# Optimization experiments

Hardware: AMD Instinct MI355X
Metric: run time of the kernel (lower is better)

The kernel has to match this reference:

```python
import jax, jax.numpy as jnp
import numpy as np

N = 100000
EPS = 1e-16

def gat_conv(x, edge_index, W, a_src, a_dst, bias, heads, out_c):
    # x: [N, F_in]; W: [F_in, heads*out_c]; a_src/a_dst: [heads, out_c]; bias: [heads*out_c]
    n = x.shape[0]
    loops = jnp.arange(n)
    src = jnp.concatenate([edge_index[0], loops])  # add self loops (PyG default)
    dst = jnp.concatenate([edge_index[1], loops])
    h = (x @ W).reshape(n, heads, out_c)                       # [N,H,C]
    s_src = jnp.sum(h * a_src[None], axis=-1)                  # [N,H]
    s_dst = jnp.sum(h * a_dst[None], axis=-1)                  # [N,H]
    e = jax.nn.leaky_relu(s_src[src] + s_dst[dst], 0.2)        # [E,H]
    m = jax.ops.segment_max(e, dst, num_segments=n)            # [N,H]
    ex = jnp.exp(e - m[dst])
    denom = jax.ops.segment_sum(ex, dst, num_segments=n)       # [N,H]
    alpha = ex / (denom[dst] + EPS)                            # [E,H]
    msg = h[src] * alpha[:, :, None]                           # [E,H,C]
    out = jax.ops.segment_sum(msg, dst, num_segments=n)        # [N,H,C]
    return out.reshape(n, heads * out_c) + bias

def setup_inputs() -> dict:
    key = jax.random.key(0)
    ks = jax.random.split(key, 10)
    num_features, num_classes, H = 512, 10, 8
    E = 3200000
    x = jax.random.normal(ks[0], (N, num_features), dtype=jnp.float32)
    edge_index = jax.random.randint(ks[1], (2, E), 0, N, dtype=jnp.int64)
    g = lambda k, shape, fan: jax.random.normal(k, shape, dtype=jnp.float32) * (1.0 / np.sqrt(fan))
    W1 = g(ks[2], (num_features, H * 8), num_features)
    a_src1 = g(ks[3], (H, 8), 8)
    a_dst1 = g(ks[4], (H, 8), 8)
    b1 = jnp.zeros((H * 8,), dtype=jnp.float32)
    W2 = g(ks[5], (H * 8, H * num_classes), H * 8)
    a_src2 = g(ks[6], (H, num_classes), num_classes)
    a_dst2 = g(ks[7], (H, num_classes), num_classes)
    b2 = jnp.zeros((H * num_classes,), dtype=jnp.float32)
    return {"x": x, "edge_index": edge_index, "W1": W1, "a_src1": a_src1,
            "a_dst1": a_dst1, "b1": b1, "W2": W2, "a_src2": a_src2,
            "a_dst2": a_dst2, "b2": b2}

def reference(x, edge_index, W1, a_src1, a_dst1, b1, W2, a_src2, a_dst2, b2):
    # inference mode: dropout = identity
    h = jax.nn.elu(gat_conv(x, edge_index, W1, a_src1, a_dst1, b1, heads=8, out_c=8))
    out = gat_conv(h, edge_index, W2, a_src2, a_dst2, b2, heads=8, out_c=10)
    return jax.nn.log_softmax(out, axis=1)
```

## Files before the change

### kernel.cpp

```cpp
#include <hip/hip_runtime.h>
#include <math.h>

#define NN 100000
#define NE 3200000
#define FIN 512
#define NH 8
#define C1 8
#define HC1 64
#define C2 10
#define HC2 80

#define EPB 4096
#define NBLK 782
#define NBUK 196
#define SCN (NBUK * NBLK)
#define SCNB 150

typedef unsigned int uint;
using bf16x8 = __attribute__((ext_vector_type(8))) short;
using f32x4  = __attribute__((ext_vector_type(4))) float;

__device__ float g_h1[NN * HC1];
__device__ float g_hact[NN * HC1];
__device__ float g_h2[NN * HC2];
__device__ uint  g_h1b[NN * 32];
__device__ uint  g_h2b[NN * 40];
__device__ uint  g_w1bt[64 * 256];
__device__ float g_ssrc[NN * NH];
__device__ float g_sdst[NN * NH];
__device__ int   g_off[NN + 1];
__device__ uint  g_pscan[SCN];
__device__ uint  g_bsum2[256];
__device__ uint  g_ebuf[NE];
__device__ int   g_csr[NE];

__device__ __forceinline__ float lrelu(float x) { return fmaxf(x, 0.2f * x); }

__device__ __forceinline__ uint bf16_rne(float x) {
  uint u = __float_as_uint(x);
  u += 0x7fffu + ((u >> 16) & 1u);
  return u >> 16;
}
__device__ __forceinline__ uint packbf2(float lo, float hi) {
  return bf16_rne(lo) | (bf16_rne(hi) << 16);
}
__device__ __forceinline__ float blo(uint v) { return __uint_as_float(v << 16); }
__device__ __forceinline__ float bhi(uint v) { return __uint_as_float(v & 0xffff0000u); }

__global__ __launch_bounds__(256) void p1count_kernel(const int* __restrict__ ei) {
  __shared__ uint cnt[NBUK];
  int tid = threadIdx.x;
  for (int i = tid; i < NBUK; i += 256) cnt[i] = 0;
  __syncthreads();
  const int* dstp = ei + NE;
  int base = blockIdx.x * EPB;
#pragma unroll 4
  for (int k = 0; k < 16; k++) {
    int e = base + k * 256 + tid;
    if (e < NE) atomicAdd(&cnt[dstp[e] >> 9], 1u);
  }
  __syncthreads();
  for (int i = tid; i < NBUK; i += 256) g_pscan[i * NBLK + blockIdx.x] = cnt[i];
}

__global__ __launch_bounds__(1024) void scn_block_kernel() {
  __shared__ uint sd[1024];
  int tid = threadIdx.x;
  int i = blockIdx.x * 1024 + tid;
  uint v = (i < SCN) ? g_pscan[i] : 0;
  sd[tid] = v;
  __syncthreads();
  for (int off = 1; off < 1024; off <<= 1) {
    uint x = (tid >= off) ? sd[tid - off] : 0;
    __syncthreads();
    sd[tid] += x;
    __syncthreads();
  }
  if (i < SCN) g_pscan[i] = sd[tid] - v;
  if (tid == 1023) g_bsum2[blockIdx.x] = sd[1023];
}

__global__ void scn_tops_kernel() {
  __shared__ uint sd[256];
  int tid = threadIdx.x;
  uint v = (tid < SCNB) ? g_bsum2[tid] : 0;
  sd[tid] = v;
  __syncthreads();
  for (int off = 1; off < 256; off <<= 1) {
    uint x = (tid >= off) ? sd[tid - off] : 0;
    __syncthreads();
    sd[tid] += x;
    __syncthreads();
  }
  g_bsum2[tid] = sd[tid] - v;
}

__global__ __launch_bounds__(1024) void scn_add_kernel() {
  int i = blockIdx.x * 1024 + threadIdx.x;
  if (i < SCN) g_pscan[i] += g_bsum2[i >> 10];
}

__global__ __launch_bounds__(256) void p1scatter_kernel(const int* __restrict__ ei) {
  __shared__ uint cur[NBUK];
  int tid = threadIdx.x;
  for (int i = tid; i < NBUK; i += 256) cur[i] = g_pscan[i * NBLK + blockIdx.x];
  __syncthreads();
  const int* srcp = ei;
  const int* dstp = ei + NE;
  int base = blockIdx.x * EPB;
#pragma unroll 4
  for (int k = 0; k < 16; k++) {
    int e = base + k * 256 + tid;
    if (e < NE) {
      int d = dstp[e], s = srcp[e];
      uint pos = atomicAdd(&cur[d >> 9], 1u);
      g_ebuf[pos] = ((uint)(d & 511) << 17) | (uint)s;
    }
  }
}

__global__ __launch_bounds__(1024) void p2build_kernel() {
  __shared__ uint hist[512];
  __shared__ uint sc[512];
  __shared__ uint cur[512];
  int tid = threadIdx.x;
  int b = blockIdx.x;
  uint bstart = g_pscan[b * NBLK];
  uint bend = (b < NBUK - 1) ? g_pscan[(b + 1) * NBLK] : NE;
  if (tid < 512) hist[tid] = 0;
  __syncthreads();
  for (uint j = bstart + tid; j < bend; j += 1024)
    atomicAdd(&hist[g_ebuf[j] >> 17], 1u);
  __syncthreads();
  uint v = (tid < 512) ? hist[tid] : 0;
  if (tid < 512) sc[tid] = v;
  __syncthreads();
  for (int off = 1; off < 512; off <<= 1) {
    uint x = (tid < 512 && tid >= off) ? sc[tid - off] : 0;
    __syncthreads();
    if (tid < 512) sc[tid] += x;
    __syncthreads();
  }
  if (tid < 512) {
    uint excl = sc[tid] - v;
    cur[tid] = excl;
    int dst = b * 512 + tid;
    if (dst < NN) g_off[dst] = (int)(bstart + excl);
  }
  if (b == NBUK - 1 && tid == 0) g_off[NN] = NE;
  __syncthreads();
  for (uint j = bstart + tid; j < bend; j += 1024) {
    uint val = g_ebuf[j];
    uint pos = bstart + atomicAdd(&cur[val >> 17], 1u);
    g_csr[pos] = (int)(val & 0x1FFFFu);
  }
}

__global__ __launch_bounds__(256) void w1cast_kernel(const float* __restrict__ W) {
  int idx = blockIdx.x * 256 + threadIdx.x;
  int n = idx & 63, kp = idx >> 6;
  float lo = W[(2 * kp) * HC1 + n];
  float hi = W[(2 * kp + 1) * HC1 + n];
  g_w1bt[n * 256 + kp] = packbf2(lo, hi);
}

__device__ __forceinline__ int sw_idx(int row, int g) {
  return row * 32 + ((g ^ (row & 7)) << 2);
}

__global__ __launch_bounds__(256) void gemm1_kernel(const float* __restrict__ X) {
  __shared__ uint sA[64 * 32];
  __shared__ uint sB[64 * 32];
  int t = threadIdx.x;
  int w = t >> 6, l = t & 63;
  int q = l >> 4, c = l & 15;
  int r0 = blockIdx.x * 64;
  int sr = t >> 2;
  int sc = t & 3;
  int xrow = r0 + sr; if (xrow >= NN) xrow = NN - 1;
  const float* xbase = &X[(long)xrow * FIN + sc * 16];
  const uint* wbase = &g_w1bt[sr * 256 + sc * 8];
  f32x4 acc[4] = {{0.f,0.f,0.f,0.f},{0.f,0.f,0.f,0.f},{0.f,0.f,0.f,0.f},{0.f,0.f,0.f,0.f}};
  for (int k0 = 0; k0 < FIN; k0 += 64) {
    __syncthreads();
    float4 f0 = *(const float4*)&xbase[k0 + 0];
    float4 f1 = *(const float4*)&xbase[k0 + 4];
    float4 f2 = *(const float4*)&xbase[k0 + 8];
    float4 f3 = *(const float4*)&xbase[k0 + 12];
    uint4 a0 = make_uint4(packbf2(f0.x, f0.y), packbf2(f0.z, f0.w),
                          packbf2(f1.x, f1.y), packbf2(f1.z, f1.w));
    uint4 a1 = make_uint4(packbf2(f2.x, f2.y), packbf2(f2.z, f2.w),
                          packbf2(f3.x, f3.y), packbf2(f3.z, f3.w));
    *(uint4*)&sA[sw_idx(sr, sc * 2 + 0)] = a0;
    *(uint4*)&sA[sw_idx(sr, sc * 2 + 1)] = a1;
    uint4 b0 = *(const uint4*)&wbase[(k0 >> 1) + 0];
    uint4 b1 = *(const uint4*)&wbase[(k0 >> 1) + 4];
    *(uint4*)&sB[sw_idx(sr, sc * 2 + 0)] = b0;
    *(uint4*)&sB[sw_idx(sr, sc * 2 + 1)] = b1;
    __syncthreads();
#pragma unroll
    for (int ks = 0; ks < 2; ks++) {
      int g = ks * 4 + q;
      bf16x8 a = *(const bf16x8*)&sA[sw_idx(w * 16 + c, g)];
#pragma unroll
      for (int nt = 0; nt < 4; nt++) {
        bf16x8 b = *(const bf16x8*)&sB[sw_idx(nt * 16 + c, g)];
        acc[nt] = __builtin_amdgcn_mfma_f32_16x16x32_bf16(a, b, acc[nt], 0, 0, 0);
      }
    }
  }
  int orow0 = r0 + w * 16 + q * 4;
#pragma unroll
  for (int nt = 0; nt < 4; nt++) {
#pragma unroll
    for (int r = 0; r < 4; r++) {
      int row = orow0 + r;
      if (row < NN) g_h1[row * HC1 + nt * 16 + c] = acc[nt][r];
    }
  }
}

template <int LAYER>
__global__ __launch_bounds__(256) void s_kernel(const float* __restrict__ a_src,
                                                const float* __restrict__ a_dst) {
  constexpr int C = (LAYER == 1) ? C1 : C2;
  const float* Hm = (LAYER == 1) ? g_h1 : g_h2;
  uint* Hb = (LAYER == 1) ? g_h1b : g_h2b;
  int t = blockIdx.x * 256 + threadIdx.x;
  if (t >= NN * NH) return;
  int h = t & 7;
  const float* row = &Hm[t * C];
  float ss = 0.f, sdd = 0.f;
  float vals[C];
#pragma unroll
  for (int c = 0; c < C; c++) {
    float v = row[c];
    vals[c] = v;
    ss = fmaf(v, a_src[h * C + c], ss);
    sdd = fmaf(v, a_dst[h * C + c], sdd);
  }
  g_ssrc[t] = ss;
  g_sdst[t] = sdd;
#pragma unroll
  for (int j = 0; j < C / 2; j++)
    Hb[t * (C / 2) + j] = packbf2(vals[2 * j], vals[2 * j + 1]);
}

__global__ __launch_bounds__(256) void agg1_kernel(const float* __restrict__ b1) {
  int gw = (blockIdx.x * 256 + threadIdx.x) >> 6;
  if (gw >= NN) return;
  int lane = threadIdx.x & 63;
  int half = lane >> 5;
  int p = lane & 31;
  int h = p >> 2;
  float sd = g_sdst[gw * NH + h];
  int begin = g_off[gw];
  int cnt = g_off[gw + 1] - begin;
  float acc0 = 0.f, acc1 = 0.f, wsum = 0.f;
  for (int j0 = 0; j0 < cnt; j0 += 64) {
    int m = cnt - j0; if (m > 64) m = 64;
    int srcv = (lane < m) ? g_csr[begin + j0 + lane] : 0;
    int j = 0;
    for (; j + 4 <= m; j += 4) {
      int sa = __shfl(srcv, j + half);
      int sb = __shfl(srcv, j + 2 + half);
      float ta = g_ssrc[sa * NH + h];
      float tb = g_ssrc[sb * NH + h];
      uint va = g_h1b[sa * 32 + p];
      uint vb = g_h1b[sb * 32 + p];
      float ea = __expf(lrelu(ta + sd));
      float eb = __expf(lrelu(tb + sd));
      acc0 = fmaf(blo(va), ea, acc0); acc1 = fmaf(bhi(va), ea, acc1);
      acc0 = fmaf(blo(vb), eb, acc0); acc1 = fmaf(bhi(vb), eb, acc1);
      wsum += ea + eb;
    }
    for (; j + 2 <= m; j += 2) {
      int s = __shfl(srcv, j + half);
      float e = __expf(lrelu(g_ssrc[s * NH + h] + sd));
      uint v = g_h1b[s * 32 + p];
      acc0 = fmaf(blo(v), e, acc0); acc1 = fmaf(bhi(v), e, acc1);
      wsum += e;
    }
    if (j < m) {
      int s = __shfl(srcv, j);
      float e = (half == 0) ? __expf(lrelu(g_ssrc[s * NH + h] + sd)) : 0.f;
      uint v = g_h1b[s * 32 + p];
      acc0 = fmaf(blo(v), e, acc0); acc1 = fmaf(bhi(v), e, acc1);
      wsum += e;
    }
  }
  acc0 += __shfl_xor(acc0, 32);
  acc1 += __shfl_xor(acc1, 32);
  wsum += __shfl_xor(wsum, 32);
  float es = __expf(lrelu(g_ssrc[gw * NH + h] + sd));
  acc0 = fmaf(g_h1[gw * HC1 + 2 * p], es, acc0);
  acc1 = fmaf(g_h1[gw * HC1 + 2 * p + 1], es, acc1);
  wsum += es;
  if (half == 0) {
    float inv = 1.f / wsum;
    float v0 = acc0 * inv + b1[2 * p];
    float v1 = acc1 * inv + b1[2 * p + 1];
    v0 = v0 > 0.f ? v0 : __expf(v0) - 1.f;
    v1 = v1 > 0.f ? v1 : __expf(v1) - 1.f;
    *(float2*)&g_hact[gw * HC1 + 2 * p] = make_float2(v0, v1);
  }
}

__global__ __launch_bounds__(256) void gemm2_kernel(const float* __restrict__ W) {
  __shared__ float sW[64 * HC2 + 64];
  int tid = threadIdx.x;
  for (int i = tid; i < 64 * HC2; i += 256) sW[i] = W[i];
  for (int i = 64 * HC2 + tid; i < 64 * HC2 + 64; i += 256) sW[i] = 0.f;
  __syncthreads();
  int lane = tid & 63;
  int w0 = (blockIdx.x * 256 + tid) >> 6;
  for (int r = w0; r < NN; r += 8192) {
    float v = g_hact[r * HC1 + lane];
    float acc0 = 0.f, acc1 = 0.f;
#pragma unroll
    for (int k = 0; k < 64; k++) {
      float xk = __shfl(v, k);
      acc0 = fmaf(xk, sW[k * HC2 + lane], acc0);
      acc1 = fmaf(xk, sW[k * HC2 + 64 + lane], acc1);
    }
    g_h2[r * HC2 + lane] = acc0;
    if (lane < 16) g_h2[r * HC2 + 64 + lane] = acc1;
  }
}

__global__ __launch_bounds__(256) void agg2_kernel(float* __restrict__ out,
                                                   const float* __restrict__ b2) {
  int gw = (blockIdx.x * 256 + threadIdx.x) >> 6;
  if (gw >= NN) return;
  int lane = threadIdx.x & 63;
  int p = lane < 40 ? lane : 39;
  int h = p / 5;
  float sd = g_sdst[gw * NH + h];
  int begin = g_off[gw];
  int cnt = g_off[gw + 1] - begin;
  float acc0 = 0.f, acc1 = 0.f, wsum = 0.f;
  for (int j0 = 0; j0 < cnt; j0 += 64) {
    int m = cnt - j0; if (m > 64) m = 64;
    int srcv = (lane < m) ? g_csr[begin + j0 + lane] : 0;
    int j = 0;
    for (; j + 4 <= m; j += 4) {
      int s0 = __shfl(srcv, j);
      int s1 = __shfl(srcv, j + 1);
      int s2 = __shfl(srcv, j + 2);
      int s3 = __shfl(srcv, j + 3);
      float t0 = g_ssrc[s0 * NH + h];
      float t1 = g_ssrc[s1 * NH + h];
      float t2 = g_ssrc[s2 * NH + h];
      float t3 = g_ssrc[s3 * NH + h];
      uint v0 = g_h2b[s0 * 40 + p];
      uint v1 = g_h2b[s1 * 40 + p];
      uint v2 = g_h2b[s2 * 40 + p];
      uint v3 = g_h2b[s3 * 40 + p];
      float e0 = __expf(lrelu(t0 + sd));
      float e1 = __expf(lrelu(t1 + sd));
      float e2 = __expf(lrelu(t2 + sd));
      float e3 = __expf(lrelu(t3 + sd));
      acc0 = fmaf(blo(v0), e0, acc0); acc1 = fmaf(bhi(v0), e0, acc1);
      acc0 = fmaf(blo(v1), e1, acc0); acc1 = fmaf(bhi(v1), e1, acc1);
      acc0 = fmaf(blo(v2), e2, acc0); acc1 = fmaf(bhi(v2), e2, acc1);
      acc0 = fmaf(blo(v3), e3, acc0); acc1 = fmaf(bhi(v3), e3, acc1);
      wsum += (e0 + e1) + (e2 + e3);
    }
    for (; j < m; j++) {
      int s = __shfl(srcv, j);
      float e = __expf(lrelu(g_ssrc[s * NH + h] + sd));
      uint v = g_h2b[s * 40 + p];
      acc0 = fmaf(blo(v), e, acc0); acc1 = fmaf(bhi(v), e, acc1);
      wsum += e;
    }
  }
  float es = __expf(lrelu(g_ssrc[gw * NH + h] + sd));
  acc0 = fmaf(g_h2[gw * HC2 + 2 * p], es, acc0);
  acc1 = fmaf(g_h2[gw * HC2 + 2 * p + 1], es, acc1);
  wsum += es;
  float inv = 1.f / wsum;
  float v0 = acc0 * inv + b2[2 * p];
  float v1 = acc1 * inv + b2[2 * p + 1];
  float mx = fmaxf(v0, v1);
  for (int o = 32; o; o >>= 1) mx = fmaxf(mx, __shfl_xor(mx, o));
  float spart = (lane < 40) ? __expf(v0 - mx) + __expf(v1 - mx) : 0.f;
  for (int o = 32; o; o >>= 1) spart += __shfl_xor(spart, o);
  float lse = mx + __logf(spart);
  if (lane < 40) *(float2*)&out[gw * HC2 + 2 * p] = make_float2(v0 - lse, v1 - lse);
}

extern "C" void kernel_launch(void* const* d_in, const int* in_sizes, int n_in,
                              void* d_out, int out_size, void* d_ws, size_t ws_size,
                              hipStream_t stream) {
  (void)in_sizes; (void)n_in; (void)out_size; (void)d_ws; (void)ws_size;
  const float* x   = (const float*)d_in[0];
  const int*   ei  = (const int*)d_in[1];
  const float* W1  = (const float*)d_in[2];
  const float* as1 = (const float*)d_in[3];
  const float* ad1 = (const float*)d_in[4];
  const float* b1  = (const float*)d_in[5];
  const float* W2  = (const float*)d_in[6];
  const float* as2 = (const float*)d_in[7];
  const float* ad2 = (const float*)d_in[8];
  const float* b2  = (const float*)d_in[9];
  float* out = (float*)d_out;

  p1count_kernel<<<NBLK, 256, 0, stream>>>(ei);
  scn_block_kernel<<<SCNB, 1024, 0, stream>>>();
  scn_tops_kernel<<<1, 256, 0, stream>>>();
  scn_add_kernel<<<SCNB, 1024, 0, stream>>>();
  p1scatter_kernel<<<NBLK, 256, 0, stream>>>(ei);
  p2build_kernel<<<NBUK, 1024, 0, stream>>>();

  w1cast_kernel<<<64, 256, 0, stream>>>(W1);
  gemm1_kernel<<<1563, 256, 0, stream>>>(x);
  s_kernel<1><<<3125, 256, 0, stream>>>(as1, ad1);
  agg1_kernel<<<25000, 256, 0, stream>>>(b1);

  gemm2_kernel<<<2048, 256, 0, stream>>>(W2);
  s_kernel<2><<<3125, 256, 0, stream>>>(as2, ad2);
  agg2_kernel<<<25000, 256, 0, stream>>>(out, b2);
}
```

Baseline: 792.5 us.

## Sort CSR neighbors by source block and use scalar index loads in aggregation

The CSR build now bins edges within each destination by the high bits of the source index, so each node's neighbor list is roughly ordered by source region for better cache locality when gathering. The aggregation kernels drop the shuffle-based 64-wide index batching and instead read each neighbor index as a wave-uniform scalar via readfirstlane. agg1 also switches to one channel per lane with 16-bit bf16 loads instead of two half-waves splitting edges. This adds a 4096-bin histogram and a larger scan in the build kernel, and it removes the cross-half reduction in agg1.

```diff
diff --git a/kernel.cpp b/kernel.cpp
--- a/kernel.cpp
+++ b/kernel.cpp
@@ -17,6 +17,7 @@
 #define SCNB 150
 
 typedef unsigned int uint;
+typedef unsigned short ushort;
 using bf16x8 = __attribute__((ext_vector_type(8))) short;
 using f32x4  = __attribute__((ext_vector_type(4))) float;
 
@@ -120,39 +121,50 @@
 }
 
 __global__ __launch_bounds__(1024) void p2build_kernel() {
-  __shared__ uint hist[512];
-  __shared__ uint sc[512];
-  __shared__ uint cur[512];
+  __shared__ uint hist[4096];
+  __shared__ uint excl[4096];
+  __shared__ uint tsum[1024];
   int tid = threadIdx.x;
   int b = blockIdx.x;
   uint bstart = g_pscan[b * NBLK];
   uint bend = (b < NBUK - 1) ? g_pscan[(b + 1) * NBLK] : NE;
-  if (tid < 512) hist[tid] = 0;
-  __syncthreads();
-  for (uint j = bstart + tid; j < bend; j += 1024)
-    atomicAdd(&hist[g_ebuf[j] >> 17], 1u);
-  __syncthreads();
-  uint v = (tid < 512) ? hist[tid] : 0;
-  if (tid < 512) sc[tid] = v;
-  __syncthreads();
-  for (int off = 1; off < 512; off <<= 1) {
-    uint x = (tid < 512 && tid >= off) ? sc[tid - off] : 0;
-    __syncthreads();
-    if (tid < 512) sc[tid] += x;
-    __syncthreads();
-  }
+  for (int i = tid; i < 4096; i += 1024) hist[i] = 0;
+  __syncthreads();
+  for (uint j = bstart + tid; j < bend; j += 1024) {
+    uint v = g_ebuf[j];
+    uint bin = ((v >> 17) << 3) | ((v & 0x1FFFFu) >> 14);
+    atomicAdd(&hist[bin], 1u);
+  }
+  __syncthreads();
+  uint h0 = hist[tid * 4 + 0], h1 = hist[tid * 4 + 1];
+  uint h2 = hist[tid * 4 + 2], h3 = hist[tid * 4 + 3];
+  uint s1 = h0 + h1, s2 = s1 + h2, s3 = s2 + h3;
+  tsum[tid] = s3;
+  __syncthreads();
+  for (int off = 1; off < 1024; off <<= 1) {
+    uint x = (tid >= off) ? tsum[tid - off] : 0;
+    __syncthreads();
+    tsum[tid] += x;
+    __syncthreads();
+  }
+  uint te = tsum[tid] - s3;
+  excl[tid * 4 + 0] = te;
+  excl[tid * 4 + 1] = te + h0;
+  excl[tid * 4 + 2] = te + s1;
+  excl[tid * 4 + 3] = te + s2;
+  __syncthreads();
   if (tid < 512) {
-    uint excl = sc[tid] - v;
-    cur[tid] = excl;
     int dst = b * 512 + tid;
-    if (dst < NN) g_off[dst] = (int)(bstart + excl);
+    if (dst < NN) g_off[dst] = (int)(bstart + excl[tid * 8]);
   }
   if (b == NBUK - 1 && tid == 0) g_off[NN] = NE;
+  for (int i = tid; i < 4096; i += 1024) hist[i] = excl[i];
   __syncthreads();
   for (uint j = bstart + tid; j < bend; j += 1024) {
-    uint val = g_ebuf[j];
-    uint pos = bstart + atomicAdd(&cur[val >> 17], 1u);
-    g_csr[pos] = (int)(val & 0x1FFFFu);
+    uint v = g_ebuf[j];
+    uint bin = ((v >> 17) << 3) | ((v & 0x1FFFFu) >> 14);
+    uint pos = bstart + atomicAdd(&hist[bin], 1u);
+    g_csr[pos] = (int)(v & 0x1FFFFu);
   }
 }
 
@@ -247,63 +259,50 @@
 }
 
 __global__ __launch_bounds__(256) void agg1_kernel(const float* __restrict__ b1) {
-  int gw = (blockIdx.x * 256 + threadIdx.x) >> 6;
+  int gw = __builtin_amdgcn_readfirstlane((int)((blockIdx.x * 256 + threadIdx.x) >> 6));
   if (gw >= NN) return;
   int lane = threadIdx.x & 63;
-  int half = lane >> 5;
-  int p = lane & 31;
-  int h = p >> 2;
+  int h = lane >> 3;
+  const ushort* __restrict__ h1u = (const ushort*)g_h1b;
   float sd = g_sdst[gw * NH + h];
   int begin = g_off[gw];
   int cnt = g_off[gw + 1] - begin;
-  float acc0 = 0.f, acc1 = 0.f, wsum = 0.f;
-  for (int j0 = 0; j0 < cnt; j0 += 64) {
-    int m = cnt - j0; if (m > 64) m = 64;
-    int srcv = (lane < m) ? g_csr[begin + j0 + lane] : 0;
-    int j = 0;
-    for (; j + 4 <= m; j += 4) {
-      int sa = __shfl(srcv, j + half);
-      int sb = __shfl(srcv, j + 2 + half);
-      float ta = g_ssrc[sa * NH + h];
-      float tb = g_ssrc[sb * NH + h];
-      uint va = g_h1b[sa * 32 + p];
-      uint vb = g_h1b[sb * 32 + p];
-      float ea = __expf(lrelu(ta + sd));
-      float eb = __expf(lrelu(tb + sd));
-      acc0 = fmaf(blo(va), ea, acc0); acc1 = fmaf(bhi(va), ea, acc1);
-      acc0 = fmaf(blo(vb), eb, acc0); acc1 = fmaf(bhi(vb), eb, acc1);
-      wsum += ea + eb;
-    }
-    for (; j + 2 <= m; j += 2) {
-      int s = __shfl(srcv, j + half);
-      float e = __expf(lrelu(g_ssrc[s * NH + h] + sd));
-      uint v = g_h1b[s * 32 + p];
-      acc0 = fmaf(blo(v), e, acc0); acc1 = fmaf(bhi(v), e, acc1);
-      wsum += e;
-    }
-    if (j < m) {
-      int s = __shfl(srcv, j);
-      float e = (half == 0) ? __expf(lrelu(g_ssrc[s * NH + h] + sd)) : 0.f;
-      uint v = g_h1b[s * 32 + p];
-      acc0 = fmaf(blo(v), e, acc0); acc1 = fmaf(bhi(v), e, acc1);
-      wsum += e;
-    }
-  }
-  acc0 += __shfl_xor(acc0, 32);
-  acc1 += __shfl_xor(acc1, 32);
-  wsum += __shfl_xor(wsum, 32);
+  float acc = 0.f, wsum = 0.f;
+  int j = 0;
+  for (; j + 4 <= cnt; j += 4) {
+    int s0 = __builtin_amdgcn_readfirstlane(g_csr[begin + j + 0]);
+    int s1 = __builtin_amdgcn_readfirstlane(g_csr[begin + j + 1]);
+    int s2 = __builtin_amdgcn_readfirstlane(g_csr[begin + j + 2]);
+    int s3 = __builtin_amdgcn_readfirstlane(g_csr[begin + j + 3]);
+    float t0 = g_ssrc[s0 * NH + h];
+    float t1 = g_ssrc[s1 * NH + h];
+    float t2 = g_ssrc[s2 * NH + h];
+    float t3 = g_ssrc[s3 * NH + h];
+    uint v0 = h1u[s0 * HC1 + lane];
+    uint v1 = h1u[s1 * HC1 + lane];
+    uint v2 = h1u[s2 * HC1 + lane];
+    uint v3 = h1u[s3 * HC1 + lane];
+    float e0 = __expf(lrelu(t0 + sd));
+    float e1 = __expf(lrelu(t1 + sd));
+    float e2 = __expf(lrelu(t2 + sd));
+    float e3 = __expf(lrelu(t3 + sd));
+    acc = fmaf(__uint_as_float(v0 << 16), e0, acc);
+    acc = fmaf(__uint_as_float(v1 << 16), e1, acc);
+    acc = fmaf(__uint_as_float(v2 << 16), e2, acc);
+    acc = fmaf(__uint_as_float(v3 << 16), e3, acc);
+    wsum += (e0 + e1) + (e2 + e3);
+  }
+  for (; j < cnt; j++) {
+    int s = __builtin_amdgcn_readfirstlane(g_csr[begin + j]);
+    float e = __expf(lrelu(g_ssrc[s * NH + h] + sd));
+    acc = fmaf(__uint_as_float((uint)h1u[s * HC1 + lane] << 16), e, acc);
+    wsum += e;
+  }
   float es = __expf(lrelu(g_ssrc[gw * NH + h] + sd));
-  acc0 = fmaf(g_h1[gw * HC1 + 2 * p], es, acc0);
-  acc1 = fmaf(g_h1[gw * HC1 + 2 * p + 1], es, acc1);
+  acc = fmaf(g_h1[gw * HC1 + lane], es, acc);
   wsum += es;
-  if (half == 0) {
-    float inv = 1.f / wsum;
-    float v0 = acc0 * inv + b1[2 * p];
-    float v1 = acc1 * inv + b1[2 * p + 1];
-    v0 = v0 > 0.f ? v0 : __expf(v0) - 1.f;
-    v1 = v1 > 0.f ? v1 : __expf(v1) - 1.f;
-    *(float2*)&g_hact[gw * HC1 + 2 * p] = make_float2(v0, v1);
-  }
+  float v = acc * (1.f / wsum) + b1[lane];
+  g_hact[gw * HC1 + lane] = v > 0.f ? v : __expf(v) - 1.f;
 }
 
 __global__ __launch_bounds__(256) void gemm2_kernel(const float* __restrict__ W) {
@@ -330,7 +329,7 @@
 
 __global__ __launch_bounds__(256) void agg2_kernel(float* __restrict__ out,
                                                    const float* __restrict__ b2) {
-  int gw = (blockIdx.x * 256 + threadIdx.x) >> 6;
+  int gw = __builtin_amdgcn_readfirstlane((int)((blockIdx.x * 256 + threadIdx.x) >> 6));
   if (gw >= NN) return;
   int lane = threadIdx.x & 63;
   int p = lane < 40 ? lane : 39;
@@ -339,40 +338,36 @@
   int begin = g_off[gw];
   int cnt = g_off[gw + 1] - begin;
   float acc0 = 0.f, acc1 = 0.f, wsum = 0.f;
-  for (int j0 = 0; j0 < cnt; j0 += 64) {
-    int m = cnt - j0; if (m > 64) m = 64;
-    int srcv = (lane < m) ? g_csr[begin + j0 + lane] : 0;
-    int j = 0;
-    for (; j + 4 <= m; j += 4) {
-      int s0 = __shfl(srcv, j);
-      int s1 = __shfl(srcv, j + 1);
-      int s2 = __shfl(srcv, j + 2);
-      int s3 = __shfl(srcv, j + 3);
-      float t0 = g_ssrc[s0 * NH + h];
-      float t1 = g_ssrc[s1 * NH + h];
-      float t2 = g_ssrc[s2 * NH + h];
-      float t3 = g_ssrc[s3 * NH + h];
-      uint v0 = g_h2b[s0 * 40 + p];
-      uint v1 = g_h2b[s1 * 40 + p];
-      uint v2 = g_h2b[s2 * 40 + p];
-      uint v3 = g_h2b[s3 * 40 + p];
-      float e0 = __expf(lrelu(t0 + sd));
-      float e1 = __expf(lrelu(t1 + sd));
-      float e2 = __expf(lrelu(t2 + sd));
-      float e3 = __expf(lrelu(t3 + sd));
-      acc0 = fmaf(blo(v0), e0, acc0); acc1 = fmaf(bhi(v0), e0, acc1);
-      acc0 = fmaf(blo(v1), e1, acc0); acc1 = fmaf(bhi(v1), e1, acc1);
-      acc0 = fmaf(blo(v2), e2, acc0); acc1 = fmaf(bhi(v2), e2, acc1);
-      acc0 = fmaf(blo(v3), e3, acc0); acc1 = fmaf(bhi(v3), e3, acc1);
-      wsum += (e0 + e1) + (e2 + e3);
-    }
-    for (; j < m; j++) {
-      int s = __shfl(srcv, j);
-      float e = __expf(lrelu(g_ssrc[s * NH + h] + sd));
-      uint v = g_h2b[s * 40 + p];
-      acc0 = fmaf(blo(v), e, acc0); acc1 = fmaf(bhi(v), e, acc1);
-      wsum += e;
-    }
+  int j = 0;
+  for (; j + 4 <= cnt; j += 4) {
+    int s0 = __builtin_amdgcn_readfirstlane(g_csr[begin + j + 0]);
+    int s1 = __builtin_amdgcn_readfirstlane(g_csr[begin + j + 1]);
+    int s2 = __builtin_amdgcn_readfirstlane(g_csr[begin + j + 2]);
+    int s3 = __builtin_amdgcn_readfirstlane(g_csr[begin + j + 3]);
+    float t0 = g_ssrc[s0 * NH + h];
+    float t1 = g_ssrc[s1 * NH + h];
+    float t2 = g_ssrc[s2 * NH + h];
+    float t3 = g_ssrc[s3 * NH + h];
+    uint v0 = g_h2b[s0 * 40 + p];
+    uint v1 = g_h2b[s1 * 40 + p];
+    uint v2 = g_h2b[s2 * 40 + p];
+    uint v3 = g_h2b[s3 * 40 + p];
+    float e0 = __expf(lrelu(t0 + sd));
+    float e1 = __expf(lrelu(t1 + sd));
+    float e2 = __expf(lrelu(t2 + sd));
+    float e3 = __expf(lrelu(t3 + sd));
+    acc0 = fmaf(blo(v0), e0, acc0); acc1 = fmaf(bhi(v0), e0, acc1);
+    acc0 = fmaf(blo(v1), e1, acc0); acc1 = fmaf(bhi(v1), e1, acc1);
+    acc0 = fmaf(blo(v2), e2, acc0); acc1 = fmaf(bhi(v2), e2, acc1);
+    acc0 = fmaf(blo(v3), e3, acc0); acc1 = fmaf(bhi(v3), e3, acc1);
+    wsum += (e0 + e1) + (e2 + e3);
+  }
+  for (; j < cnt; j++) {
+    int s = __builtin_amdgcn_readfirstlane(g_csr[begin + j]);
+    float e = __expf(lrelu(g_ssrc[s * NH + h] + sd));
+    uint v = g_h2b[s * 40 + p];
+    acc0 = fmaf(blo(v), e, acc0); acc1 = fmaf(bhi(v), e, acc1);
+    wsum += e;
   }
   float es = __expf(lrelu(g_ssrc[gw * NH + h] + sd));
   acc0 = fmaf(g_h2[gw * HC2 + 2 * p], es, acc0);
```

Measured after the change: 785.0 us. No clear change (-1.0%).
